# Kernel tuning notes

Hardware: AMD Instinct MI355X
Metric: run time of the kernel (lower is better)

## Reference

```python
import jax, jax.numpy as jnp
import numpy as np

NEG = -1e30  # log-space 'zero' that keeps gradients finite (vs -inf)


def setup_inputs() -> dict:
    key = jax.random.key(0)
    k1, k2, k3, k4 = jax.random.split(key, 4)
    B, T, V, S = 32, 2048, 128, 256
    predictions = jax.random.normal(k1, (B, T, V), dtype=jnp.float32)
    # input lengths in [T//2, T]; target lengths in [S//4, S]; labels in [1, V) (0 is blank)
    prediction_lengths = jax.random.randint(k2, (B,), T // 2, T + 1, dtype=jnp.int32)
    ground_truths = jax.random.randint(k3, (B, S), 1, V, dtype=jnp.int32)
    ground_truth_lengths = jax.random.randint(k4, (B,), S // 4, S + 1, dtype=jnp.int32)
    return {
        "predictions": predictions,
        "prediction_lengths": prediction_lengths,
        "ground_truths": ground_truths,
        "ground_truth_lengths": ground_truth_lengths,
    }


def _ctc_loss(log_probs, targets, input_lengths, target_lengths, blank=0):
    # log_probs: [T, B, V]; targets: [B, S]
    T, B, V = log_probs.shape
    S = targets.shape[1]
    L = 2 * S + 1  # extended label sequence: blank, l1, blank, l2, ..., blank
    ext = jnp.full((B, L), blank, dtype=targets.dtype).at[:, 1::2].set(targets)
    # skip transition s-2 -> s allowed iff ext[s] != blank and ext[s] != ext[s-2]
    skip = jnp.concatenate(
        [jnp.zeros((B, 2), dtype=bool), (ext[:, 2:] != blank) & (ext[:, 2:] != ext[:, :-2])],
        axis=1,
    )
    # gather per-extended-label log-probs: [T, B, L]
    lp_ext = jnp.take_along_axis(log_probs, jnp.broadcast_to(ext[None], (T, B, L)), axis=2)

    alpha0 = (
        jnp.full((B, L), NEG, dtype=log_probs.dtype)
        .at[:, 0].set(lp_ext[0, :, 0])
        .at[:, 1].set(lp_ext[0, :, 1])
    )

    def step(alpha, lp_t):
        a1 = alpha
        a2 = jnp.pad(alpha[:, :-1], ((0, 0), (1, 0)), constant_values=NEG)
        a3 = jnp.where(skip, jnp.pad(alpha[:, :-2], ((0, 0), (2, 0)), constant_values=NEG), NEG)
        m = jnp.maximum(jnp.maximum(a1, a2), a3)
        new = m + jnp.log(jnp.exp(a1 - m) + jnp.exp(a2 - m) + jnp.exp(a3 - m)) + lp_t
        return new, new

    _, alphas = jax.lax.scan(step, alpha0, lp_ext[1:])
    alphas = jnp.concatenate([alpha0[None], alphas], axis=0)  # [T, B, L]

    bidx = jnp.arange(B)
    alpha_final = alphas[input_lengths - 1, bidx]  # [B, L] at each sequence's last frame
    last = 2 * target_lengths  # index of final blank; last-1 is final label
    loss = -jnp.logaddexp(alpha_final[bidx, last], alpha_final[bidx, last - 1])
    loss = jnp.where(loss < 1e10, loss, 0.0)  # zero_infinity=True
    # torch reduction='mean': per-sample loss / target_length, then batch mean
    return (loss / target_lengths.astype(loss.dtype)).mean()


def reference(predictions, prediction_lengths, ground_truths, ground_truth_lengths):
    # module: transpose to [T, B, V], log_softmax over vocab, then CTC loss
    log_probs = jax.nn.log_softmax(jnp.transpose(predictions, (1, 0, 2)), axis=2)
    return _ctc_loss(log_probs, ground_truths, prediction_lengths, ground_truth_lengths, blank=0)
```

## Files before the change

kernel.cpp:

```cpp
#include <hip/hip_runtime.h>
#include <math.h>

constexpr int V = 128;

__device__ __forceinline__ double dpp_shr1_f64(double x) {
    int lo = __builtin_amdgcn_update_dpp(0, __double2loint(x), 0x138, 0xf, 0xf, false);
    int hi = __builtin_amdgcn_update_dpp(0, __double2hiint(x), 0x138, 0xf, 0xf, false);
    return __hiloint2double(hi, lo);
}
__device__ __forceinline__ double dpp_shl1_f64(double x) {
    int lo = __builtin_amdgcn_update_dpp(0, __double2loint(x), 0x130, 0xf, 0xf, false);
    int hi = __builtin_amdgcn_update_dpp(0, __double2hiint(x), 0x130, 0xf, 0xf, false);
    return __hiloint2double(hi, lo);
}

__device__ __forceinline__ unsigned f32_to_bf16_rne(float f) {
    unsigned u = __float_as_uint(f);
    return (u + 0x7fffu + ((u >> 16) & 1u)) >> 16;
}

__global__ __launch_bounds__(256) void ctc_prelude(
    const float* __restrict__ pred, const int* __restrict__ gt,
    const int* __restrict__ gt_len, const int* __restrict__ pred_len,
    char* __restrict__ g16, float* __restrict__ z, int* __restrict__ flags,
    int T, int S)
{
    if (blockIdx.x == 0 && threadIdx.x < 65) flags[threadIdx.x] = 0;

    int wid  = blockIdx.x * 4 + (threadIdx.x >> 6);
    int lane = threadIdx.x & 63;
    int w4   = threadIdx.x >> 6;
    int b    = wid / T;
    int t    = wid - b * T;
    if (t >= pred_len[b]) return;
    __shared__ float rows[4][V];

    const float2* p = (const float2*)pred + (size_t)wid * 64;
    float2 v = p[lane];
    rows[w4][2 * lane]     = v.x;
    rows[w4][2 * lane + 1] = v.y;
    float x0 = __shfl(v.x, 0, 64);
    float s = __expf(v.x) + __expf(v.y);
    #pragma unroll
    for (int off = 32; off >= 1; off >>= 1) s += __shfl_xor(s, off, 64);
    if (lane == 0) z[wid] = __logf(s) - v.x;

    int4 la = *(const int4*)(gt + b * S + 4 * lane);
    int tl = gt_len[b];
    float4 o;
    o.x = (4 * lane + 0 < tl) ? __expf(rows[w4][la.x] - x0) : 0.f;
    o.y = (4 * lane + 1 < tl) ? __expf(rows[w4][la.y] - x0) : 0.f;
    o.z = (4 * lane + 2 < tl) ? __expf(rows[w4][la.z] - x0) : 0.f;
    o.w = (4 * lane + 3 < tl) ? __expf(rows[w4][la.w] - x0) : 0.f;

    uint2 w;
    w.x = f32_to_bf16_rne(o.x) | (f32_to_bf16_rne(o.y) << 16);
    w.y = f32_to_bf16_rne(o.z) | (f32_to_bf16_rne(o.w) << 16);
    *(uint2*)(g16 + (size_t)wid * 512 + lane * 8) = w;
}

__global__ __launch_bounds__(64, 1) void ctc_scan_bi(
    const char*  __restrict__ g16,
    const int*   __restrict__ pred_len,
    const int*   __restrict__ gt,
    const int*   __restrict__ gt_len,
    const float* __restrict__ z,
    double*      __restrict__ fwdv,
    double*      __restrict__ bwdv,
    int*         __restrict__ Kf,
    int*         __restrict__ Kb,
    int* done, int* gdone, float* lossb,
    float* __restrict__ out,
    int T, int S, int B)
{
    const int blk  = blockIdx.x;
    const int b    = blk >> 1;
    const int dir  = blk & 1;
    const int lane = threadIdx.x;
    const int len  = pred_len[b];
    const int tl   = gt_len[b];
    const int L    = 2 * tl + 1;
    const int m    = (len + 1) >> 1;

    int4 la = *(const int4*)(gt + b * S + 4 * lane);
    int law_up = __shfl_up(la.w, 1, 64);
    int lax_dn = __shfl_down(la.x, 1, 64);
    const double sk0 = (lane > 0 && la.x != law_up) ? 1.0 : 0.0;
    const double sk1 = (la.y != la.x) ? 1.0 : 0.0;
    const double sk2 = (la.z != la.y) ? 1.0 : 0.0;
    const double sk3 = (la.w != la.z) ? 1.0 : 0.0;
    const double sk4 = (lax_dn != la.w) ? 1.0 : 0.0;

    const char* gb = g16 + (size_t)b * T * 512 + lane * 8;

    uint2 raw[32];
    double u[9];
    int K = 0;

    auto RESCALE = [&]() {
        double mx = u[0];
        #pragma unroll
        for (int j = 1; j < 9; ++j) mx = fmax(mx, u[j]);
        #pragma unroll
        for (int off = 32; off >= 1; off >>= 1)
            mx = fmax(mx, __shfl_xor(mx, off, 64));
        int k = ((__double2hiint(mx) >> 20) & 0x7ff) - 1023;
        #pragma unroll
        for (int j = 0; j < 9; ++j) u[j] = ldexp(u[j], -k);
        K += k;
    };

    if (dir == 0) {
        #pragma unroll
        for (int i = 0; i < 32; ++i)
            raw[i] = *(const uint2*)(gb + (size_t)i * 512);
        #pragma unroll
        for (int j = 0; j < 9; ++j) u[j] = 0.0;
        if (lane == 0) {
            u[0] = 1.0;
            u[1] = (double)__uint_as_float(raw[0].x << 16);
        }
        raw[0] = *(const uint2*)(gb + (size_t)32 * 512);
        const char* pf = gb + (size_t)33 * 512;

        auto FSTEP = [&](int i) {
            uint2 q = raw[i];
            raw[i] = *(const uint2*)pf; pf += 512;
            double um1 = dpp_shr1_f64(u[7]);
            double gx = (double)__uint_as_float(q.x << 16);
            double gy = (double)__uint_as_float(q.x & 0xffff0000u);
            double gz = (double)__uint_as_float(q.y << 16);
            double gw = (double)__uint_as_float(q.y & 0xffff0000u);
            u[8] = u[8] + u[7];
            u[7] = (fma(sk3, u[5], u[6]) + u[7]) * gw;
            u[6] = u[6] + u[5];
            u[5] = (fma(sk2, u[3], u[4]) + u[5]) * gz;
            u[4] = u[4] + u[3];
            u[3] = (fma(sk1, u[1], u[2]) + u[3]) * gy;
            u[2] = u[2] + u[1];
            u[1] = (fma(sk0, um1, u[0]) + u[1]) * gx;
            u[0] = u[0] + um1;
        };

        #pragma unroll
        for (int t = 1; t < 32; ++t) FSTEP(t);
        RESCALE();
        int tb = 32;
        for (; tb + 32 <= m; tb += 32) {
            #pragma unroll
            for (int i = 0; i < 32; ++i) FSTEP(i);
            if (((tb + 32) & 63) == 0) RESCALE();
        }
        #pragma unroll
        for (int i = 0; i < 31; ++i)
            if (tb + i < m) FSTEP(i);
        RESCALE();

        double* outv = fwdv + (size_t)b * 520;
        #pragma unroll
        for (int j = 0; j < 8; ++j) outv[8 * lane + j] = u[j];
        if (lane == 63) outv[512] = u[8];
        if (lane == 0)  Kf[b] = K;
    } else {
        const int nb = len - m;
        #pragma unroll
        for (int i = 0; i < 32; ++i)
            raw[i] = *(const uint2*)(gb + (size_t)(len - 1 - i) * 512);
        #pragma unroll
        for (int j = 0; j < 8; ++j) {
            int s = 8 * lane + j;
            u[j] = (s == 2 * tl || s == 2 * tl - 1) ? 1.0 : 0.0;
        }
        u[8] = (lane == 63 && L == 513) ? 1.0 : 0.0;
        const char* pf = gb + (size_t)(len - 33) * 512;

        auto BSTEP = [&](int i) {
            uint2 q = raw[i];
            raw[i] = *(const uint2*)pf; pf -= 512;
            double d0 = dpp_shl1_f64(u[0]);
            if (lane == 63) d0 = u[8];
            double gx = (double)__uint_as_float(q.x << 16);
            double gy = (double)__uint_as_float(q.x & 0xffff0000u);
            double gz = (double)__uint_as_float(q.y << 16);
            double gw = (double)__uint_as_float(q.y & 0xffff0000u);
            double p1 = gx * u[1], p3 = gy * u[3];
            double p5 = gz * u[5], p7 = gw * u[7];
            double dp = dpp_shl1_f64(p1);
            u[0] = u[0] + p1;
            u[1] = fma(sk1, p3, u[2]) + p1;
            u[2] = u[2] + p3;
            u[3] = fma(sk2, p5, u[4]) + p3;
            u[4] = u[4] + p5;
            u[5] = fma(sk3, p7, u[6]) + p5;
            u[6] = u[6] + p7;
            u[7] = fma(sk4, dp, d0) + p7;
        };

        #pragma unroll
        for (int k = 0; k < 32; ++k) BSTEP(k);
        RESCALE();
        int kb = 32;
        for (; kb + 32 <= nb; kb += 32) {
            #pragma unroll
            for (int i = 0; i < 32; ++i) BSTEP(i);
            if (((kb + 32) & 63) == 0) RESCALE();
        }
        #pragma unroll
        for (int i = 0; i < 31; ++i)
            if (kb + i < nb) BSTEP(i);
        RESCALE();

        double* outv = bwdv + (size_t)b * 520;
        #pragma unroll
        for (int j = 0; j < 8; ++j) outv[8 * lane + j] = u[j];
        if (lane == 63) outv[512] = u[8];
        if (lane == 0)  Kb[b] = K;
    }

    __threadfence();
    int prev = 0;
    if (lane == 0)
        prev = __hip_atomic_fetch_add(&done[b], 1, __ATOMIC_ACQ_REL,
                                      __HIP_MEMORY_SCOPE_AGENT);
    prev = __shfl(prev, 0, 64);
    if (prev == 0) return;
    __threadfence();

    const double* f = fwdv + (size_t)b * 520;
    const double* w = bwdv + (size_t)b * 520;
    double c = 0.0;
    #pragma unroll
    for (int j = 0; j < 8; ++j)
        c = fma(f[8 * lane + j], w[8 * lane + j], c);
    if (lane == 63) c = fma(f[512], w[512], c);
    #pragma unroll
    for (int off = 32; off >= 1; off >>= 1) c += __shfl_xor(c, off, 64);

    double zs = 0.0;
    const float* zb = z + b * T;
    int t = lane;
    for (; t + 448 < len; t += 512) {
        float a0 = zb[t],       a1 = zb[t + 64],  a2 = zb[t + 128];
        float a3 = zb[t + 192], a4 = zb[t + 256], a5 = zb[t + 320];
        float a6 = zb[t + 384], a7 = zb[t + 448];
        zs += (((double)a0 + a1) + ((double)a2 + a3))
            + (((double)a4 + a5) + ((double)a6 + a7));
    }
    for (; t < len; t += 64) zs += (double)zb[t];
    #pragma unroll
    for (int off = 32; off >= 1; off >>= 1) zs += __shfl_xor(zs, off, 64);

    if (lane == 0) {
        double logp = log(c)
                    + (double)(Kf[b] + Kb[b]) * 0.6931471805599453 - zs;
        double loss = -logp;
        if (!(loss < 1e10)) loss = 0.0;
        if (loss < 0.0)     loss = 0.0;
        lossb[b] = (float)(loss / (double)tl);
        __threadfence();
        int pg = __hip_atomic_fetch_add(gdone, 1, __ATOMIC_ACQ_REL,
                                        __HIP_MEMORY_SCOPE_AGENT);
        if (pg == B - 1) {
            __threadfence();
            float ssum = 0.0f;
            for (int i = 0; i < B; ++i) ssum += lossb[i];
            out[0] = ssum / (float)B;
        }
    }
}

constexpr int SPL  = 9;
constexpr int RING = 32;

__global__ void ctc_reduce_kernel(const float* __restrict__ ls,
                                  float* __restrict__ out, int B)
{
    if (blockIdx.x == 0 && threadIdx.x == 0) {
        float s = 0.0f;
        for (int i = 0; i < B; ++i) s += ls[i];
        out[0] = s / (float)B;
    }
}

__global__ __launch_bounds__(256) void softmax_z_kernel(
    const float* __restrict__ pred, float* __restrict__ z, int nrows)
{
    int w    = blockIdx.x * 4 + (threadIdx.x >> 6);
    int lane = threadIdx.x & 63;
    if (w >= nrows) return;
    const float2* p = (const float2*)pred;
    float2 v = p[(size_t)w * 64 + lane];
    float s = __expf(v.x) + __expf(v.y);
    #pragma unroll
    for (int off = 32; off >= 1; off >>= 1) s += __shfl_xor(s, off, 64);
    if (lane == 0) z[w] = __logf(s);
}

__device__ __forceinline__ void ctc_step_fb(
    const float* __restrict__ rowbase, const int* __restrict__ goff,
    const double* __restrict__ skd, double (&u)[SPL], int lane)
{
    float gf[SPL];
    #pragma unroll
    for (int j = 0; j < SPL; ++j)
        gf[j] = *(const float*)((const char*)rowbase + goff[j]);
    double um1 = __shfl_up(u[8], 1, 64);
    double um2 = __shfl_up(u[7], 1, 64);
    if (lane == 0) { um1 = 0.0; um2 = 0.0; }
    #pragma unroll
    for (int jj = 0; jj < SPL; ++jj) {
        int j = SPL - 1 - jj;
        double a2 = (j >= 1) ? u[j - 1] : um1;
        double a3 = (j >= 2) ? u[j - 2] : ((j == 1) ? um1 : um2);
        double t  = fma(skd[j], a3, a2) + u[j];
        u[j] = t * (double)gf[j];
    }
}

__device__ __forceinline__ void ctc_rescale_fb(double (&u)[SPL], int& K)
{
    double m = u[0];
    #pragma unroll
    for (int j = 1; j < SPL; ++j) m = fmax(m, u[j]);
    #pragma unroll
    for (int off = 32; off >= 1; off >>= 1) m = fmax(m, __shfl_xor(m, off, 64));
    if (m > 0.0) {
        int e = (__double2hiint(m) >> 20) & 0x7ff;
        int k = e - 1023;
        #pragma unroll
        for (int j = 0; j < SPL; ++j) u[j] = ldexp(u[j], -k);
        K += k;
    }
}

__global__ __launch_bounds__(64) void ctc_scan_kernel(
    const float* __restrict__ pred, const int* __restrict__ pred_len,
    const int* __restrict__ gt, const int* __restrict__ gt_len,
    const float* __restrict__ z, float* __restrict__ loss_out, int T, int S)
{
    const int b    = blockIdx.x;
    const int lane = threadIdx.x;
    const int len  = pred_len[b];
    const int tl   = gt_len[b];
    const int L    = 2 * tl + 1;

    __shared__ float ring[RING][V];
    __shared__ int   gts[512];

    for (int i = lane; i < S; i += 64) gts[i] = gt[b * S + i];
    __syncthreads();

    int    goff[SPL];
    double skd[SPL];
    #pragma unroll
    for (int j = 0; j < SPL; ++j) {
        int s = SPL * lane + j;
        int e = 0, ep = 0;
        if (s < L && (s & 1)) e = gts[s >> 1];
        if (s >= 2 && s < L && (s & 1)) ep = gts[(s - 2) >> 1];
        goff[j] = e * 4;
        skd[j]  = (s >= 2 && s < L && e != 0 && e != ep) ? 1.0 : 0.0;
    }

    const float2* rowp = (const float2*)(pred + (size_t)b * T * V);
    float2 raw[16];

    #pragma unroll
    for (int i = 0; i < 16; ++i) raw[i] = rowp[(size_t)i * 64 + lane];
    #pragma unroll
    for (int i = 0; i < 16; ++i) {
        float2 w; w.x = __expf(raw[i].x); w.y = __expf(raw[i].y);
        *(float2*)&ring[i][2 * lane] = w;
    }
    #pragma unroll
    for (int i = 0; i < 16; ++i) raw[i] = rowp[(size_t)(16 + i) * 64 + lane];
    #pragma unroll
    for (int i = 0; i < 16; ++i) {
        float2 w; w.x = __expf(raw[i].x); w.y = __expf(raw[i].y);
        *(float2*)&ring[16 + i][2 * lane] = w;
    }
    #pragma unroll
    for (int i = 0; i < 16; ++i) {
        int r = 32 + i; if (r > T - 1) r = T - 1;
        raw[i] = rowp[(size_t)r * 64 + lane];
    }

    double u[SPL];
    #pragma unroll
    for (int j = 0; j < SPL; ++j) {
        int s = SPL * lane + j;
        float w0 = *(const float*)((const char*)&ring[0][0] + goff[j]);
        u[j] = (s < 2) ? (double)w0 : 0.0;
    }
    int K = 0;

    for (int t = 1; t < 16 && t < len; ++t)
        ctc_step_fb(&ring[t & (RING - 1)][0], goff, skd, u, lane);
    ctc_rescale_fb(u, K);

    int tb = 16;
    for (; tb + 16 <= len; tb += 16) {
        #pragma unroll
        for (int i = 0; i < 16; ++i) {
            float2 w; w.x = __expf(raw[i].x); w.y = __expf(raw[i].y);
            *(float2*)&ring[(tb + 16 + i) & (RING - 1)][2 * lane] = w;
        }
        #pragma unroll
        for (int i = 0; i < 16; ++i) {
            int r = tb + 32 + i; if (r > T - 1) r = T - 1;
            raw[i] = rowp[(size_t)r * 64 + lane];
        }
        #pragma unroll
        for (int i = 0; i < 16; ++i)
            ctc_step_fb(&ring[(tb + i) & (RING - 1)][0], goff, skd, u, lane);
        ctc_rescale_fb(u, K);
    }

    for (int t = tb; t < len; ++t)
        ctc_step_fb(&ring[t & (RING - 1)][0], goff, skd, u, lane);

    double contrib = 0.0;
    #pragma unroll
    for (int j = 0; j < SPL; ++j) {
        int s = SPL * lane + j;
        if (s == L - 1 || s == L - 2) contrib += u[j];
    }
    #pragma unroll
    for (int off = 32; off >= 1; off >>= 1)
        contrib += __shfl_xor(contrib, off, 64);

    double zsum = 0.0;
    for (int t = lane; t < len; t += 64) zsum += (double)z[b * T + t];
    #pragma unroll
    for (int off = 32; off >= 1; off >>= 1)
        zsum += __shfl_xor(zsum, off, 64);

    if (lane == 0) {
        double lg    = log(contrib);
        double alpha = lg + (double)K * 0.6931471805599453 - zsum;
        double loss  = -alpha;
        if (!(loss < 1e10)) loss = 0.0;
        loss_out[b] = (float)(loss / (double)tl);
    }
}

extern "C" void kernel_launch(void* const* d_in, const int* in_sizes, int n_in,
                              void* d_out, int out_size, void* d_ws, size_t ws_size,
                              hipStream_t stream) {
    const float* pred = (const float*)d_in[0];
    const int*   plen = (const int*)d_in[1];
    const int*   gts  = (const int*)d_in[2];
    const int*   glen = (const int*)d_in[3];

    const int B = in_sizes[1];
    const int S = in_sizes[2] / B;
    const int T = in_sizes[0] / (B * V);
    const size_t BT = (size_t)B * T;

    float* out = (float*)d_out;
    char*  ws  = (char*)d_ws;

    size_t off_fl  = 0;
    size_t off_z   = 1024;
    size_t off_fw  = (off_z + BT * 4 + 255) & ~(size_t)255;
    size_t off_bw  = off_fw  + (size_t)B * 520 * 8;
    size_t off_kf  = off_bw  + (size_t)B * 520 * 8;
    size_t off_kb  = off_kf  + (size_t)B * 4;
    size_t off_g   = (off_kb + (size_t)B * 4 + 1023) & ~(size_t)1023;
    size_t need    = off_g + BT * 512;

    bool fast_ok = (ws_size >= need) && (S == 256) && (T % 4 == 0) &&
                   (T >= 128) && (B >= 1) && (B <= 64);

    if (fast_ok) {
        int*    flags = (int*)(ws + off_fl);
        int*    done  = flags;
        int*    gdone = flags + 64;
        float*  lossb = (float*)(ws + off_fl + 512);
        float*  zp    = (float*)(ws + off_z);
        double* fw    = (double*)(ws + off_fw);
        double* bw    = (double*)(ws + off_bw);
        int*    kf    = (int*)(ws + off_kf);
        int*    kb    = (int*)(ws + off_kb);
        char*   g16   = ws + off_g;

        ctc_prelude<<<B * T / 4, 256, 0, stream>>>(pred, gts, glen, plen,
                                                   g16, zp, flags, T, S);
        ctc_scan_bi<<<2 * B, 64, 0, stream>>>(g16, plen, gts, glen, zp,
                                              fw, bw, kf, kb,
                                              done, gdone, lossb, out, T, S, B);
    } else {
        float* zbuf = (float*)ws;
        float* lb   = zbuf + BT;
        int nrows = B * T;
        softmax_z_kernel<<<(nrows + 3) / 4, 256, 0, stream>>>(pred, zbuf, nrows);
        ctc_scan_kernel<<<B, 64, 0, stream>>>(pred, plen, gts, glen, zbuf, lb, T, S);
        ctc_reduce_kernel<<<1, 64, 0, stream>>>(lb, out, B);
    }
}
```

Before: 168.0 us.

## Split CTC scan into producer and consumer waves with an LDS double-buffered ring

The scan block now has two waves. Wave 1 loads 32-row chunks of the bf16 emission table from global memory into a double-buffered LDS ring, and wave 0 runs the serial forward or backward recurrence, reading from LDS with a short register prefetch. The goal is to take global-load latency and the 32-entry register staging array off the latency-bound recurrence wave. In exchange, a __syncthreads is paid every 32 steps and LDS reads replace register-resident data, which could stall the recurrence if the barrier cost outweighs the latency saved.

Measured after the change: 167.9 us. No clear change (-0.0%).

```diff
diff --git a/kernel.cpp b/kernel.cpp
--- a/kernel.cpp
+++ b/kernel.cpp
@@ -59,7 +59,7 @@
     *(uint2*)(g16 + (size_t)wid * 512 + lane * 8) = w;
 }
 
-__global__ __launch_bounds__(64, 1) void ctc_scan_bi(
+__global__ __launch_bounds__(128, 1) void ctc_scan_bi(
     const char*  __restrict__ g16,
     const int*   __restrict__ pred_len,
     const int*   __restrict__ gt,
@@ -76,11 +76,14 @@
     const int blk  = blockIdx.x;
     const int b    = blk >> 1;
     const int dir  = blk & 1;
-    const int lane = threadIdx.x;
+    const int wv   = threadIdx.x >> 6;
+    const int lane = threadIdx.x & 63;
     const int len  = pred_len[b];
     const int tl   = gt_len[b];
     const int L    = 2 * tl + 1;
     const int m    = (len + 1) >> 1;
+
+    __shared__ uint2 ring[2][32][64];
 
     int4 la = *(const int4*)(gt + b * S + 4 * lane);
     int law_up = __shfl_up(la.w, 1, 64);
@@ -93,7 +96,6 @@
 
     const char* gb = g16 + (size_t)b * T * 512 + lane * 8;
 
-    uint2 raw[32];
     double u[9];
     int K = 0;
 
@@ -110,112 +112,165 @@
         K += k;
     };
 
+    auto FSTEP_Q = [&](uint2 q) {
+        double um1 = dpp_shr1_f64(u[7]);
+        double gx = (double)__uint_as_float(q.x << 16);
+        double gy = (double)__uint_as_float(q.x & 0xffff0000u);
+        double gz = (double)__uint_as_float(q.y << 16);
+        double gw = (double)__uint_as_float(q.y & 0xffff0000u);
+        u[8] = u[8] + u[7];
+        u[7] = (fma(sk3, u[5], u[6]) + u[7]) * gw;
+        u[6] = u[6] + u[5];
+        u[5] = (fma(sk2, u[3], u[4]) + u[5]) * gz;
+        u[4] = u[4] + u[3];
+        u[3] = (fma(sk1, u[1], u[2]) + u[3]) * gy;
+        u[2] = u[2] + u[1];
+        u[1] = (fma(sk0, um1, u[0]) + u[1]) * gx;
+        u[0] = u[0] + um1;
+    };
+
+    auto BSTEP_Q = [&](uint2 q) {
+        double d0 = dpp_shl1_f64(u[0]);
+        if (lane == 63) d0 = u[8];
+        double gx = (double)__uint_as_float(q.x << 16);
+        double gy = (double)__uint_as_float(q.x & 0xffff0000u);
+        double gz = (double)__uint_as_float(q.y << 16);
+        double gw = (double)__uint_as_float(q.y & 0xffff0000u);
+        double p1 = gx * u[1], p3 = gy * u[3];
+        double p5 = gz * u[5], p7 = gw * u[7];
+        double dp = dpp_shl1_f64(p1);
+        u[0] = u[0] + p1;
+        u[1] = fma(sk1, p3, u[2]) + p1;
+        u[2] = u[2] + p3;
+        u[3] = fma(sk2, p5, u[4]) + p3;
+        u[4] = u[4] + p5;
+        u[5] = fma(sk3, p7, u[6]) + p5;
+        u[6] = u[6] + p7;
+        u[7] = fma(sk4, dp, d0) + p7;
+    };
+
+    auto PRODUCE = [&](int buf, int r0, int stride ) {
+        uint2 tmp[16];
+        #pragma unroll
+        for (int j = 0; j < 16; ++j)
+            tmp[j] = *(const uint2*)(gb + (size_t)(r0 + stride * j) * 512);
+        #pragma unroll
+        for (int j = 0; j < 16; ++j) ring[buf][j][lane] = tmp[j];
+        #pragma unroll
+        for (int j = 0; j < 16; ++j)
+            tmp[j] = *(const uint2*)(gb + (size_t)(r0 + stride * (16 + j)) * 512);
+        #pragma unroll
+        for (int j = 0; j < 16; ++j) ring[buf][16 + j][lane] = tmp[j];
+    };
+
     if (dir == 0) {
         #pragma unroll
-        for (int i = 0; i < 32; ++i)
-            raw[i] = *(const uint2*)(gb + (size_t)i * 512);
-        #pragma unroll
         for (int j = 0; j < 9; ++j) u[j] = 0.0;
-        if (lane == 0) {
-            u[0] = 1.0;
-            u[1] = (double)__uint_as_float(raw[0].x << 16);
-        }
-        raw[0] = *(const uint2*)(gb + (size_t)32 * 512);
-        const char* pf = gb + (size_t)33 * 512;
-
-        auto FSTEP = [&](int i) {
-            uint2 q = raw[i];
-            raw[i] = *(const uint2*)pf; pf += 512;
-            double um1 = dpp_shr1_f64(u[7]);
-            double gx = (double)__uint_as_float(q.x << 16);
-            double gy = (double)__uint_as_float(q.x & 0xffff0000u);
-            double gz = (double)__uint_as_float(q.y << 16);
-            double gw = (double)__uint_as_float(q.y & 0xffff0000u);
-            u[8] = u[8] + u[7];
-            u[7] = (fma(sk3, u[5], u[6]) + u[7]) * gw;
-            u[6] = u[6] + u[5];
-            u[5] = (fma(sk2, u[3], u[4]) + u[5]) * gz;
-            u[4] = u[4] + u[3];
-            u[3] = (fma(sk1, u[1], u[2]) + u[3]) * gy;
-            u[2] = u[2] + u[1];
-            u[1] = (fma(sk0, um1, u[0]) + u[1]) * gx;
-            u[0] = u[0] + um1;
-        };
-
-        #pragma unroll
-        for (int t = 1; t < 32; ++t) FSTEP(t);
-        RESCALE();
-        int tb = 32;
-        for (; tb + 32 <= m; tb += 32) {
+        const int nrows = m;
+        const int nch = (nrows + 31) >> 5;
+        for (int it = 0; it <= nch; ++it) {
+            if (wv == 1 && it < nch)
+                PRODUCE(it & 1, it << 5, +1);
+            if (wv == 0 && it >= 1) {
+                int c = it - 1;
+                int buf = c & 1;
+                uint2 rr[4];
+                #pragma unroll
+                for (int j = 0; j < 4; ++j) rr[j] = ring[buf][j][lane];
+                if (c == 0) {
+                    if (lane == 0) {
+                        u[0] = 1.0;
+                        u[1] = (double)__uint_as_float(rr[0].x << 16);
+                    }
+                    rr[0] = ring[buf][4][lane];
+                    #pragma unroll
+                    for (int i = 1; i < 32; ++i) {
+                        uint2 q = rr[i & 3];
+                        if (i + 4 < 32) rr[i & 3] = ring[buf][i + 4][lane];
+                        FSTEP_Q(q);
+                    }
+                } else if (((c + 1) << 5) <= nrows) {
+                    #pragma unroll
+                    for (int i = 0; i < 32; ++i) {
+                        uint2 q = rr[i & 3];
+                        if (i + 4 < 32) rr[i & 3] = ring[buf][i + 4][lane];
+                        FSTEP_Q(q);
+                    }
+                } else {
+                    int rem = nrows - (c << 5);
+                    #pragma unroll
+                    for (int i = 0; i < 32; ++i) {
+                        if (i < rem) {
+                            uint2 q = rr[i & 3];
+                            if (i + 4 < 32) rr[i & 3] = ring[buf][i + 4][lane];
+                            FSTEP_Q(q);
+                        }
+                    }
+                }
+                if (c & 1) RESCALE();
+            }
+            __syncthreads();
+        }
+        if (wv == 0) {
+            RESCALE();
+            double* outv = fwdv + (size_t)b * 520;
             #pragma unroll
-            for (int i = 0; i < 32; ++i) FSTEP(i);
-            if (((tb + 32) & 63) == 0) RESCALE();
-        }
-        #pragma unroll
-        for (int i = 0; i < 31; ++i)
-            if (tb + i < m) FSTEP(i);
-        RESCALE();
-
-        double* outv = fwdv + (size_t)b * 520;
-        #pragma unroll
-        for (int j = 0; j < 8; ++j) outv[8 * lane + j] = u[j];
-        if (lane == 63) outv[512] = u[8];
-        if (lane == 0)  Kf[b] = K;
+            for (int j = 0; j < 8; ++j) outv[8 * lane + j] = u[j];
+            if (lane == 63) outv[512] = u[8];
+            if (lane == 0)  Kf[b] = K;
+        }
     } else {
         const int nb = len - m;
-        #pragma unroll
-        for (int i = 0; i < 32; ++i)
-            raw[i] = *(const uint2*)(gb + (size_t)(len - 1 - i) * 512);
         #pragma unroll
         for (int j = 0; j < 8; ++j) {
             int s = 8 * lane + j;
             u[j] = (s == 2 * tl || s == 2 * tl - 1) ? 1.0 : 0.0;
         }
         u[8] = (lane == 63 && L == 513) ? 1.0 : 0.0;
-        const char* pf = gb + (size_t)(len - 33) * 512;
-
-        auto BSTEP = [&](int i) {
-            uint2 q = raw[i];
-            raw[i] = *(const uint2*)pf; pf -= 512;
-            double d0 = dpp_shl1_f64(u[0]);
-            if (lane == 63) d0 = u[8];
-            double gx = (double)__uint_as_float(q.x << 16);
-            double gy = (double)__uint_as_float(q.x & 0xffff0000u);
-            double gz = (double)__uint_as_float(q.y << 16);
-            double gw = (double)__uint_as_float(q.y & 0xffff0000u);
-            double p1 = gx * u[1], p3 = gy * u[3];
-            double p5 = gz * u[5], p7 = gw * u[7];
-            double dp = dpp_shl1_f64(p1);
-            u[0] = u[0] + p1;
-            u[1] = fma(sk1, p3, u[2]) + p1;
-            u[2] = u[2] + p3;
-            u[3] = fma(sk2, p5, u[4]) + p3;
-            u[4] = u[4] + p5;
-            u[5] = fma(sk3, p7, u[6]) + p5;
-            u[6] = u[6] + p7;
-            u[7] = fma(sk4, dp, d0) + p7;
-        };
-
-        #pragma unroll
-        for (int k = 0; k < 32; ++k) BSTEP(k);
-        RESCALE();
-        int kb = 32;
-        for (; kb + 32 <= nb; kb += 32) {
+        const int nrows = nb;
+        const int nch = (nrows + 31) >> 5;
+        for (int it = 0; it <= nch; ++it) {
+            if (wv == 1 && it < nch)
+                PRODUCE(it & 1, len - 1 - (it << 5), -1);
+            if (wv == 0 && it >= 1) {
+                int c = it - 1;
+                int buf = c & 1;
+                uint2 rr[4];
+                #pragma unroll
+                for (int j = 0; j < 4; ++j) rr[j] = ring[buf][j][lane];
+                if (((c + 1) << 5) <= nrows) {
+                    #pragma unroll
+                    for (int i = 0; i < 32; ++i) {
+                        uint2 q = rr[i & 3];
+                        if (i + 4 < 32) rr[i & 3] = ring[buf][i + 4][lane];
+                        BSTEP_Q(q);
+                    }
+                } else {
+                    int rem = nrows - (c << 5);
+                    #pragma unroll
+                    for (int i = 0; i < 32; ++i) {
+                        if (i < rem) {
+                            uint2 q = rr[i & 3];
+                            if (i + 4 < 32) rr[i & 3] = ring[buf][i + 4][lane];
+                            BSTEP_Q(q);
+                        }
+                    }
+                }
+                if (c & 1) RESCALE();
+            }
+            __syncthreads();
+        }
+        if (wv == 0) {
+            RESCALE();
+            double* outv = bwdv + (size_t)b * 520;
             #pragma unroll
-            for (int i = 0; i < 32; ++i) BSTEP(i);
-            if (((kb + 32) & 63) == 0) RESCALE();
-        }
-        #pragma unroll
-        for (int i = 0; i < 31; ++i)
-            if (kb + i < nb) BSTEP(i);
-        RESCALE();
-
-        double* outv = bwdv + (size_t)b * 520;
-        #pragma unroll
-        for (int j = 0; j < 8; ++j) outv[8 * lane + j] = u[j];
-        if (lane == 63) outv[512] = u[8];
-        if (lane == 0)  Kb[b] = K;
-    }
+            for (int j = 0; j < 8; ++j) outv[8 * lane + j] = u[j];
+            if (lane == 63) outv[512] = u[8];
+            if (lane == 0)  Kb[b] = K;
+        }
+    }
+
+    if (wv != 0) return;
 
     __threadfence();
     int prev = 0;
@@ -486,9 +541,9 @@
 
         ctc_prelude<<<B * T / 4, 256, 0, stream>>>(pred, gts, glen, plen,
                                                    g16, zp, flags, T, S);
-        ctc_scan_bi<<<2 * B, 64, 0, stream>>>(g16, plen, gts, glen, zp,
-                                              fw, bw, kf, kb,
-                                              done, gdone, lossb, out, T, S, B);
+        ctc_scan_bi<<<2 * B, 128, 0, stream>>>(g16, plen, gts, glen, zp,
+                                               fw, bw, kf, kb,
+                                               done, gdone, lossb, out, T, S, B);
     } else {
         float* zbuf = (float*)ws;
         float* lb   = zbuf + BT;
```

## Interleave forward and backward CTC recursions within a single wavefront per batch

Applied to the files above, without the earlier changes.

Instead of launching two blocks per sample (one forward, one backward) that meet through global memory, scratch buffers and an atomic handshake, one 64-lane block now runs both recursions in the same loop with interleaved steps. The combine then uses the register-resident alpha and beta directly, which removes the global writes, the fence and the atomic. Interleaving two independent dependency chains should hide ALU and DPP latency in a latency-bound serial scan. The prefetch ring per direction shrinks from 32 to 16 entries to keep register pressure in check, and the launch halves to B blocks, so half as many CUs are busy.

Result: slower. 225.0 us (+33.9%).

```diff
diff --git a/kernel.cpp b/kernel.cpp
--- a/kernel.cpp
+++ b/kernel.cpp
@@ -47,15 +47,14 @@
 
     int4 la = *(const int4*)(gt + b * S + 4 * lane);
     int tl = gt_len[b];
-    float4 o;
-    o.x = (4 * lane + 0 < tl) ? __expf(rows[w4][la.x] - x0) : 0.f;
-    o.y = (4 * lane + 1 < tl) ? __expf(rows[w4][la.y] - x0) : 0.f;
-    o.z = (4 * lane + 2 < tl) ? __expf(rows[w4][la.z] - x0) : 0.f;
-    o.w = (4 * lane + 3 < tl) ? __expf(rows[w4][la.w] - x0) : 0.f;
+    float o0 = (4 * lane + 0 < tl) ? __expf(rows[w4][la.x] - x0) : 0.f;
+    float o1 = (4 * lane + 1 < tl) ? __expf(rows[w4][la.y] - x0) : 0.f;
+    float o2 = (4 * lane + 2 < tl) ? __expf(rows[w4][la.z] - x0) : 0.f;
+    float o3 = (4 * lane + 3 < tl) ? __expf(rows[w4][la.w] - x0) : 0.f;
 
     uint2 w;
-    w.x = f32_to_bf16_rne(o.x) | (f32_to_bf16_rne(o.y) << 16);
-    w.y = f32_to_bf16_rne(o.z) | (f32_to_bf16_rne(o.w) << 16);
+    w.x = f32_to_bf16_rne(o0) | (f32_to_bf16_rne(o1) << 16);
+    w.y = f32_to_bf16_rne(o2) | (f32_to_bf16_rne(o3) << 16);
     *(uint2*)(g16 + (size_t)wid * 512 + lane * 8) = w;
 }
 
@@ -65,22 +64,17 @@
     const int*   __restrict__ gt,
     const int*   __restrict__ gt_len,
     const float* __restrict__ z,
-    double*      __restrict__ fwdv,
-    double*      __restrict__ bwdv,
-    int*         __restrict__ Kf,
-    int*         __restrict__ Kb,
-    int* done, int* gdone, float* lossb,
+    int* gdone, float* lossb,
     float* __restrict__ out,
     int T, int S, int B)
 {
-    const int blk  = blockIdx.x;
-    const int b    = blk >> 1;
-    const int dir  = blk & 1;
+    const int b    = blockIdx.x;
     const int lane = threadIdx.x;
     const int len  = pred_len[b];
     const int tl   = gt_len[b];
     const int L    = 2 * tl + 1;
     const int m    = (len + 1) >> 1;
+    const int nb   = len - m;
 
     int4 la = *(const int4*)(gt + b * S + 4 * lane);
     int law_up = __shfl_up(la.w, 1, 64);
@@ -93,146 +87,121 @@
 
     const char* gb = g16 + (size_t)b * T * 512 + lane * 8;
 
-    uint2 raw[32];
-    double u[9];
-    int K = 0;
-
-    auto RESCALE = [&]() {
-        double mx = u[0];
-        #pragma unroll
-        for (int j = 1; j < 9; ++j) mx = fmax(mx, u[j]);
+    uint2  rawf[16], rawb[16];
+    double uf[9], ub[9];
+    int Kf = 0, Kb = 0;
+
+    auto RESCALE_F = [&]() {
+        double mx = uf[0];
+        #pragma unroll
+        for (int j = 1; j < 9; ++j) mx = fmax(mx, uf[j]);
         #pragma unroll
         for (int off = 32; off >= 1; off >>= 1)
             mx = fmax(mx, __shfl_xor(mx, off, 64));
         int k = ((__double2hiint(mx) >> 20) & 0x7ff) - 1023;
         #pragma unroll
-        for (int j = 0; j < 9; ++j) u[j] = ldexp(u[j], -k);
-        K += k;
+        for (int j = 0; j < 9; ++j) uf[j] = ldexp(uf[j], -k);
+        Kf += k;
     };
-
-    if (dir == 0) {
-        #pragma unroll
-        for (int i = 0; i < 32; ++i)
-            raw[i] = *(const uint2*)(gb + (size_t)i * 512);
-        #pragma unroll
-        for (int j = 0; j < 9; ++j) u[j] = 0.0;
-        if (lane == 0) {
-            u[0] = 1.0;
-            u[1] = (double)__uint_as_float(raw[0].x << 16);
-        }
-        raw[0] = *(const uint2*)(gb + (size_t)32 * 512);
-        const char* pf = gb + (size_t)33 * 512;
-
-        auto FSTEP = [&](int i) {
-            uint2 q = raw[i];
-            raw[i] = *(const uint2*)pf; pf += 512;
-            double um1 = dpp_shr1_f64(u[7]);
-            double gx = (double)__uint_as_float(q.x << 16);
-            double gy = (double)__uint_as_float(q.x & 0xffff0000u);
-            double gz = (double)__uint_as_float(q.y << 16);
-            double gw = (double)__uint_as_float(q.y & 0xffff0000u);
-            u[8] = u[8] + u[7];
-            u[7] = (fma(sk3, u[5], u[6]) + u[7]) * gw;
-            u[6] = u[6] + u[5];
-            u[5] = (fma(sk2, u[3], u[4]) + u[5]) * gz;
-            u[4] = u[4] + u[3];
-            u[3] = (fma(sk1, u[1], u[2]) + u[3]) * gy;
-            u[2] = u[2] + u[1];
-            u[1] = (fma(sk0, um1, u[0]) + u[1]) * gx;
-            u[0] = u[0] + um1;
-        };
-
-        #pragma unroll
-        for (int t = 1; t < 32; ++t) FSTEP(t);
-        RESCALE();
-        int tb = 32;
-        for (; tb + 32 <= m; tb += 32) {
-            #pragma unroll
-            for (int i = 0; i < 32; ++i) FSTEP(i);
-            if (((tb + 32) & 63) == 0) RESCALE();
-        }
-        #pragma unroll
-        for (int i = 0; i < 31; ++i)
-            if (tb + i < m) FSTEP(i);
-        RESCALE();
-
-        double* outv = fwdv + (size_t)b * 520;
-        #pragma unroll
-        for (int j = 0; j < 8; ++j) outv[8 * lane + j] = u[j];
-        if (lane == 63) outv[512] = u[8];
-        if (lane == 0)  Kf[b] = K;
-    } else {
-        const int nb = len - m;
-        #pragma unroll
-        for (int i = 0; i < 32; ++i)
-            raw[i] = *(const uint2*)(gb + (size_t)(len - 1 - i) * 512);
-        #pragma unroll
-        for (int j = 0; j < 8; ++j) {
-            int s = 8 * lane + j;
-            u[j] = (s == 2 * tl || s == 2 * tl - 1) ? 1.0 : 0.0;
-        }
-        u[8] = (lane == 63 && L == 513) ? 1.0 : 0.0;
-        const char* pf = gb + (size_t)(len - 33) * 512;
-
-        auto BSTEP = [&](int i) {
-            uint2 q = raw[i];
-            raw[i] = *(const uint2*)pf; pf -= 512;
-            double d0 = dpp_shl1_f64(u[0]);
-            if (lane == 63) d0 = u[8];
-            double gx = (double)__uint_as_float(q.x << 16);
-            double gy = (double)__uint_as_float(q.x & 0xffff0000u);
-            double gz = (double)__uint_as_float(q.y << 16);
-            double gw = (double)__uint_as_float(q.y & 0xffff0000u);
-            double p1 = gx * u[1], p3 = gy * u[3];
-            double p5 = gz * u[5], p7 = gw * u[7];
-            double dp = dpp_shl1_f64(p1);
-            u[0] = u[0] + p1;
-            u[1] = fma(sk1, p3, u[2]) + p1;
-            u[2] = u[2] + p3;
-            u[3] = fma(sk2, p5, u[4]) + p3;
-            u[4] = u[4] + p5;
-            u[5] = fma(sk3, p7, u[6]) + p5;
-            u[6] = u[6] + p7;
-            u[7] = fma(sk4, dp, d0) + p7;
-        };
-
-        #pragma unroll
-        for (int k = 0; k < 32; ++k) BSTEP(k);
-        RESCALE();
-        int kb = 32;
-        for (; kb + 32 <= nb; kb += 32) {
-            #pragma unroll
-            for (int i = 0; i < 32; ++i) BSTEP(i);
-            if (((kb + 32) & 63) == 0) RESCALE();
-        }
-        #pragma unroll
-        for (int i = 0; i < 31; ++i)
-            if (kb + i < nb) BSTEP(i);
-        RESCALE();
-
-        double* outv = bwdv + (size_t)b * 520;
-        #pragma unroll
-        for (int j = 0; j < 8; ++j) outv[8 * lane + j] = u[j];
-        if (lane == 63) outv[512] = u[8];
-        if (lane == 0)  Kb[b] = K;
-    }
-
-    __threadfence();
-    int prev = 0;
-    if (lane == 0)
-        prev = __hip_atomic_fetch_add(&done[b], 1, __ATOMIC_ACQ_REL,
-                                      __HIP_MEMORY_SCOPE_AGENT);
-    prev = __shfl(prev, 0, 64);
-    if (prev == 0) return;
-    __threadfence();
-
-    const double* f = fwdv + (size_t)b * 520;
-    const double* w = bwdv + (size_t)b * 520;
+    auto RESCALE_B = [&]() {
+        double mx = ub[0];
+        #pragma unroll
+        for (int j = 1; j < 9; ++j) mx = fmax(mx, ub[j]);
+        #pragma unroll
+        for (int off = 32; off >= 1; off >>= 1)
+            mx = fmax(mx, __shfl_xor(mx, off, 64));
+        int k = ((__double2hiint(mx) >> 20) & 0x7ff) - 1023;
+        #pragma unroll
+        for (int j = 0; j < 9; ++j) ub[j] = ldexp(ub[j], -k);
+        Kb += k;
+    };
+
+    #pragma unroll
+    for (int i = 0; i < 16; ++i)
+        rawf[i] = *(const uint2*)(gb + (size_t)i * 512);
+    #pragma unroll
+    for (int j = 0; j < 9; ++j) uf[j] = 0.0;
+    if (lane == 0) {
+        uf[0] = 1.0;
+        uf[1] = (double)__uint_as_float(rawf[0].x << 16);
+    }
+    rawf[0] = *(const uint2*)(gb + (size_t)16 * 512);
+    const char* pff = gb + (size_t)17 * 512;
+
+    #pragma unroll
+    for (int i = 0; i < 16; ++i)
+        rawb[i] = *(const uint2*)(gb + (size_t)(len - 1 - i) * 512);
+    #pragma unroll
+    for (int j = 0; j < 8; ++j) {
+        int s = 8 * lane + j;
+        ub[j] = (s == 2 * tl || s == 2 * tl - 1) ? 1.0 : 0.0;
+    }
+    ub[8] = (lane == 63 && L == 513) ? 1.0 : 0.0;
+    const char* pfb = gb + (size_t)(len - 17) * 512;
+
+    auto FSTEP = [&](int i) {
+        uint2 q = rawf[i];
+        rawf[i] = *(const uint2*)pff; pff += 512;
+        double um1 = dpp_shr1_f64(uf[7]);
+        double gx = (double)__uint_as_float(q.x << 16);
+        double gy = (double)__uint_as_float(q.x & 0xffff0000u);
+        double gz = (double)__uint_as_float(q.y << 16);
+        double gw = (double)__uint_as_float(q.y & 0xffff0000u);
+        uf[8] = uf[8] + uf[7];
+        uf[7] = (fma(sk3, uf[5], uf[6]) + uf[7]) * gw;
+        uf[6] = uf[6] + uf[5];
+        uf[5] = (fma(sk2, uf[3], uf[4]) + uf[5]) * gz;
+        uf[4] = uf[4] + uf[3];
+        uf[3] = (fma(sk1, uf[1], uf[2]) + uf[3]) * gy;
+        uf[2] = uf[2] + uf[1];
+        uf[1] = (fma(sk0, um1, uf[0]) + uf[1]) * gx;
+        uf[0] = uf[0] + um1;
+    };
+
+    auto BSTEP = [&](int i) {
+        uint2 q = rawb[i];
+        rawb[i] = *(const uint2*)pfb; pfb -= 512;
+        double d0 = dpp_shl1_f64(ub[0]);
+        if (lane == 63) d0 = ub[8];
+        double gx = (double)__uint_as_float(q.x << 16);
+        double gy = (double)__uint_as_float(q.x & 0xffff0000u);
+        double gz = (double)__uint_as_float(q.y << 16);
+        double gw = (double)__uint_as_float(q.y & 0xffff0000u);
+        double p1 = gx * ub[1], p3 = gy * ub[3];
+        double p5 = gz * ub[5], p7 = gw * ub[7];
+        double dp = dpp_shl1_f64(p1);
+        ub[0] = ub[0] + p1;
+        ub[1] = fma(sk1, p3, ub[2]) + p1;
+        ub[2] = ub[2] + p3;
+        ub[3] = fma(sk2, p5, ub[4]) + p3;
+        ub[4] = ub[4] + p5;
+        ub[5] = fma(sk3, p7, ub[6]) + p5;
+        ub[6] = ub[6] + p7;
+        ub[7] = fma(sk4, dp, d0) + p7;
+    };
+
+    #pragma unroll
+    for (int i = 0; i < 16; ++i) {
+        if (i >= 1) FSTEP(i);
+        BSTEP(i);
+    }
+    int tb = 16, kb = 16;
+    for (; kb + 16 <= nb; tb += 16, kb += 16) {
+        #pragma unroll
+        for (int i = 0; i < 16; ++i) { FSTEP(i); BSTEP(i); }
+        if (((kb + 16) & 63) == 0) { RESCALE_F(); RESCALE_B(); }
+    }
+    #pragma unroll
+    for (int i = 0; i < 16; ++i) {
+        if (tb + i < m)  FSTEP(i);
+        if (kb + i < nb) BSTEP(i);
+    }
+    RESCALE_F(); RESCALE_B();
+
     double c = 0.0;
     #pragma unroll
-    for (int j = 0; j < 8; ++j)
-        c = fma(f[8 * lane + j], w[8 * lane + j], c);
-    if (lane == 63) c = fma(f[512], w[512], c);
+    for (int j = 0; j < 8; ++j) c = fma(uf[j], ub[j], c);
+    if (lane == 63) c = fma(uf[8], ub[8], c);
     #pragma unroll
     for (int off = 32; off >= 1; off >>= 1) c += __shfl_xor(c, off, 64);
 
@@ -252,7 +221,7 @@
 
     if (lane == 0) {
         double logp = log(c)
-                    + (double)(Kf[b] + Kb[b]) * 0.6931471805599453 - zs;
+                    + (double)(Kf + Kb) * 0.6931471805599453 - zs;
         double loss = -logp;
         if (!(loss < 1e10)) loss = 0.0;
         if (loss < 0.0)     loss = 0.0;
@@ -460,35 +429,25 @@
     float* out = (float*)d_out;
     char*  ws  = (char*)d_ws;
 
-    size_t off_fl  = 0;
-    size_t off_z   = 1024;
-    size_t off_fw  = (off_z + BT * 4 + 255) & ~(size_t)255;
-    size_t off_bw  = off_fw  + (size_t)B * 520 * 8;
-    size_t off_kf  = off_bw  + (size_t)B * 520 * 8;
-    size_t off_kb  = off_kf  + (size_t)B * 4;
-    size_t off_g   = (off_kb + (size_t)B * 4 + 1023) & ~(size_t)1023;
-    size_t need    = off_g + BT * 512;
+    size_t off_fl = 0;
+    size_t off_z  = 1024;
+    size_t off_g  = (off_z + BT * 4 + 1023) & ~(size_t)1023;
+    size_t need   = off_g + BT * 512;
 
     bool fast_ok = (ws_size >= need) && (S == 256) && (T % 4 == 0) &&
-                   (T >= 128) && (B >= 1) && (B <= 64);
+                   (T >= 96) && (B >= 1) && (B <= 64);
 
     if (fast_ok) {
         int*    flags = (int*)(ws + off_fl);
-        int*    done  = flags;
         int*    gdone = flags + 64;
         float*  lossb = (float*)(ws + off_fl + 512);
         float*  zp    = (float*)(ws + off_z);
-        double* fw    = (double*)(ws + off_fw);
-        double* bw    = (double*)(ws + off_bw);
-        int*    kf    = (int*)(ws + off_kf);
-        int*    kb    = (int*)(ws + off_kb);
         char*   g16   = ws + off_g;
 
         ctc_prelude<<<B * T / 4, 256, 0, stream>>>(pred, gts, glen, plen,
                                                    g16, zp, flags, T, S);
-        ctc_scan_bi<<<2 * B, 64, 0, stream>>>(g16, plen, gts, glen, zp,
-                                              fw, bw, kf, kb,
-                                              done, gdone, lossb, out, T, S, B);
+        ctc_scan_bi<<<B, 64, 0, stream>>>(g16, plen, gts, glen, zp,
+                                          gdone, lossb, out, T, S, B);
     } else {
         float* zbuf = (float*)ws;
         float* lb   = zbuf + BT;
```
